# Performance work log

Hardware: AMD Instinct MI355X
Metric: run time of the kernel (lower is better)

Reference implementation:

```python
import jax, jax.numpy as jnp
import numpy as np

N_QUBITS = 12
N_LAYERS = 3
FEAT_DIM = 64
BATCH = 8192
PI = float(np.pi)


def setup_inputs() -> dict:
    key = jax.random.key(0)
    k1, k2, k3 = jax.random.split(key, 3)
    x = jax.random.normal(k1, (BATCH, FEAT_DIM), dtype=jnp.float32)
    # nn.Linear(feature_dim, num_qubits, bias=False) weight: [num_qubits, feature_dim]
    W = jax.random.normal(k2, (N_QUBITS, FEAT_DIM), dtype=jnp.float32) * (1.0 / np.sqrt(FEAT_DIM))
    # quantum params ~ Uniform(-pi, pi), shape [num_layers, num_qubits, 2] (RY, RZ angles)
    quantum_params = jax.random.uniform(k3, (N_LAYERS, N_QUBITS, 2), minval=-PI, maxval=PI, dtype=jnp.float32)
    return {"x": x, "W": W, "quantum_params": quantum_params}


def _halves(st, ax):
    a0 = jax.lax.index_in_dim(st, 0, ax, keepdims=True)
    a1 = jax.lax.index_in_dim(st, 1, ax, keepdims=True)
    return a0, a1


def _ry(st, theta, q, n):
    # RY(t) = [[cos t/2, -sin t/2], [sin t/2, cos t/2]] on qubit q (wire 0 = most significant)
    ax = q + 1
    c = jnp.cos(theta * 0.5)
    s = jnp.sin(theta * 0.5)
    if jnp.ndim(c) > 0:  # per-batch angles -> broadcast [B,1,...,1]
        c = c.reshape(c.shape + (1,) * n)
        s = s.reshape(s.shape + (1,) * n)
    a0, a1 = _halves(st, ax)
    return jnp.concatenate([c * a0 - s * a1, s * a0 + c * a1], axis=ax)


def _rz(st, theta, q, n):
    # RZ(t) = diag(e^{-i t/2}, e^{i t/2}) on qubit q
    ax = q + 1
    ph = jnp.exp(-0.5j * theta)
    a0, a1 = _halves(st, ax)
    return jnp.concatenate([ph * a0, jnp.conj(ph) * a1], axis=ax)


def _cnot(st, ctrl, tgt):
    # flip target amplitudes on the control=1 subspace
    ax_c, ax_t = ctrl + 1, tgt + 1
    s0, s1 = _halves(st, ax_c)
    return jnp.concatenate([s0, jnp.flip(s1, axis=ax_t)], axis=ax_c)


def reference(x, W, quantum_params):
    n = N_QUBITS
    # feature projection + tanh squashing to [-pi, pi]
    angles = jnp.tanh(x @ W.T) * PI  # [B, n]
    B = x.shape[0]
    # batched state vector |0...0>, shape [B] + [2]*n (wire 0 most significant, PennyLane convention)
    st = jnp.zeros((B,) + (2,) * n, dtype=jnp.complex64)
    st = st.at[(slice(None),) + (0,) * n].set(1.0)
    for layer in range(N_LAYERS):
        # data (re)uploading: RY(features[i]) each layer since data_reuploading=True
        for q in range(n):
            st = _ry(st, angles[:, q], q, n)
        # variational rotations
        for q in range(n):
            st = _ry(st, quantum_params[layer, q, 0], q, n)
            st = _rz(st, quantum_params[layer, q, 1], q, n)
        # ring entanglement
        for q in range(n):
            st = _cnot(st, q, (q + 1) % n)
    probs = jnp.real(st * jnp.conj(st))  # [B] + [2]*n
    outs = []
    for q in range(n):  # <PauliZ_q> = p(bit_q=0) - p(bit_q=1)
        axes = tuple(a for a in range(1, n + 1) if a != q + 1)
        p = probs.sum(axis=axes)  # [B, 2]
        outs.append(p[:, 0] - p[:, 1])
    return jnp.stack(outs, axis=1).astype(x.dtype)  # [B, n]
```

## Files before the change

kernel.cpp:

```cpp
#include <hip/hip_runtime.h>

namespace {

constexpr int NQ = 12;
constexpr int NL = 3;
constexpr int FEAT = 64;
constexpr float PI_F = 3.14159265358979323846f;

typedef float f2 __attribute__((ext_vector_type(2)));

struct Maps {
  unsigned m[NL][NQ];
  unsigned rv[NL][NQ];
  unsigned rf[NQ];
  bool ok;
};

constexpr Maps compute_raw() {
  Maps mp{};
  unsigned col[NQ] = {}, row[NQ] = {};
  for (int b = 0; b < NQ; ++b) { col[b] = 1u << b; row[b] = 1u << b; }
  mp.ok = true;
  for (int L = 0; L < NL; ++L) {
    for (int q = 0; q < NQ; ++q) {
      mp.m[L][q]  = col[NQ - 1 - q];
      mp.rv[L][q] = row[NQ - 1 - q];
      unsigned x = mp.m[L][q] & mp.rv[L][q];
      int pc = 0;
      for (int i = 0; i < NQ; ++i) pc ^= (int)((x >> i) & 1u);
      if (pc != 1) mp.ok = false;
    }
    for (int q = 0; q < NQ; ++q) {
      int bc = NQ - 1 - q;
      int bt = NQ - 1 - ((q + 1) % NQ);
      col[bc] ^= col[bt];
      row[bt] ^= row[bc];
    }
  }
  for (int q = 0; q < NQ; ++q) mp.rf[q] = row[NQ - 1 - q];
  return mp;
}

constexpr int pc12(unsigned x) { int c = 0; for (int i = 0; i < 12; ++i) c += (int)((x >> i) & 1u); return c; }

constexpr unsigned pmask(unsigned m, const int* pos) {
  unsigned r = 0;
  for (int b = 0; b < 12; ++b) if ((m >> b) & 1u) r |= 1u << pos[b];
  return r;
}

constexpr Maps compute_maps() {
  Maps raw = compute_raw();
  unsigned bestS = 0xFC0u; int best = -1;
  for (unsigned S = 0; S < 4096; ++S) {
    if (pc12(S) != 6) continue;
    int cnt = 0;
    for (int L = 0; L < NL; ++L)
      for (int q = 0; q < NQ; ++q)
        if ((raw.m[L][q] & ~S) == 0u) ++cnt;
    if (cnt > best) { best = cnt; bestS = S; }
  }
  int pos[12] = {};
  int lo = 0, hi = 6;
  for (int b = 0; b < 12; ++b) {
    if ((bestS >> b) & 1u) pos[b] = hi++; else pos[b] = lo++;
  }
  Maps mp{};
  mp.ok = raw.ok;
  for (int L = 0; L < NL; ++L)
    for (int q = 0; q < NQ; ++q) {
      mp.m[L][q]  = pmask(raw.m[L][q], pos);
      mp.rv[L][q] = pmask(raw.rv[L][q], pos);
    }
  for (int q = 0; q < NQ; ++q) mp.rf[q] = pmask(raw.rf[q], pos);
  return mp;
}

constexpr Maps MP = compute_maps();
static_assert(MP.ok, "pairing invariant violated");

__device__ __forceinline__ f2 pk_mul_bl(f2 a, f2 u) {
  f2 d;
  asm("v_pk_mul_f32 %0, %1, %2 op_sel:[0,0] op_sel_hi:[1,0]" : "=v"(d) : "v"(a), "v"(u));
  return d;
}
__device__ __forceinline__ f2 pk_fma_rot_p(f2 a, f2 u, f2 c) {
  f2 d;
  asm("v_pk_fma_f32 %0, %1, %2, %3 op_sel:[1,1,0] op_sel_hi:[0,1,1] neg_lo:[1,0,0]"
      : "=v"(d) : "v"(a), "v"(u), "v"(c));
  return d;
}
__device__ __forceinline__ f2 pk_fma_rot_m(f2 a, f2 u, f2 c) {
  f2 d;
  asm("v_pk_fma_f32 %0, %1, %2, %3 op_sel:[1,1,0] op_sel_hi:[0,1,1] neg_hi:[1,0,0]"
      : "=v"(d) : "v"(a), "v"(u), "v"(c));
  return d;
}
__device__ __forceinline__ f2 pk_fma_bl_p(f2 p, f2 v, f2 c) {
  f2 d;
  asm("v_pk_fma_f32 %0, %1, %2, %3 op_sel:[0,0,0] op_sel_hi:[1,0,1]"
      : "=v"(d) : "v"(p), "v"(v), "v"(c));
  return d;
}
__device__ __forceinline__ f2 pk_fma_bl_m(f2 p, f2 v, f2 c) {
  f2 d;
  asm("v_pk_fma_f32 %0, %1, %2, %3 op_sel:[0,0,0] op_sel_hi:[1,0,1] neg_lo:[0,1,0] neg_hi:[0,1,0]"
      : "=v"(d) : "v"(p), "v"(v), "v"(c));
  return d;
}
__device__ __forceinline__ f2 pk_mul_d(f2 a, f2 b) {
  f2 d;
  asm("v_pk_mul_f32 %0, %1, %2" : "=v"(d) : "v"(a), "v"(b));
  return d;
}
__device__ __forceinline__ f2 pk_fma_d(f2 a, f2 b, f2 c) {
  f2 d;
  asm("v_pk_fma_f32 %0, %1, %2, %3" : "=v"(d) : "v"(a), "v"(b), "v"(c));
  return d;
}

template<bool REAL>
__device__ __forceinline__ f2 updp(f2 a, f2 p, f2 u, f2 v) {
  if constexpr (REAL) return pk_fma_bl_p(p, v, pk_mul_bl(a, u));
  else return pk_fma_rot_p(p, v, pk_fma_bl_p(p, v, pk_fma_rot_p(a, u, pk_mul_bl(a, u))));
}
template<bool REAL>
__device__ __forceinline__ f2 updm(f2 a, f2 p, f2 u, f2 v) {
  if constexpr (REAL) return pk_fma_bl_m(p, v, pk_mul_bl(a, u));
  else return pk_fma_rot_p(p, v, pk_fma_bl_m(p, v, pk_fma_rot_m(a, u, pk_mul_bl(a, u))));
}

template<unsigned MLO>
__device__ __forceinline__ float shx(float v, int lane4) {
  if constexpr (MLO == 0u) {
    return v;
  } else if constexpr (MLO < 32u) {
    constexpr int off = (int)((MLO << 10) | 0x1fu);
    return __int_as_float(__builtin_amdgcn_ds_swizzle(__float_as_int(v), off));
  } else {
    int addr = lane4 ^ (int)(MLO << 2);
    return __int_as_float(__builtin_amdgcn_ds_bpermute(addr, __float_as_int(v)));
  }
}

template<unsigned M, unsigned R, int NREG, bool REAL>
__device__ __forceinline__ void gate(f2* st, float ghalf, float phihalf, int lane, int lane4) {
  float s, c;
  __sincosf(ghalf, &s, &c);
  constexpr unsigned MHI = (M >> 6) & 63u;
  constexpr unsigned MLO = M & 63u;
  constexpr unsigned RHI = (R >> 6) & 63u;
  constexpr unsigned RLO = R & 63u;
  float sL = (__popc((int)(RLO & (unsigned)lane)) & 1) ? -1.f : 1.f;
  f2 u, v;
  if constexpr (REAL) {
    u.x = c;       u.y = 0.f;
    v.x = -s * sL; v.y = 0.f;
  } else {
    float sf, cf;
    __sincosf(phihalf, &sf, &cf);
    u.x = c * cf;         u.y = (-c * sf) * sL;
    v.x = (-s * cf) * sL; v.y = s * sf;
  }
  if constexpr (MLO == 0u) {
    constexpr unsigned TB = MHI & (~MHI + 1u);
    #pragma unroll
    for (int r = 0; r < NREG; ++r) {
      if ((r & (int)TB) == 0) {
        int r2 = r ^ (int)MHI;
        const bool rp = ((__builtin_popcount((unsigned)r & RHI)) & 1) != 0;
        f2 a = st[r], b = st[r2];
        st[r]  = rp ? updm<REAL>(a, b, u, v) : updp<REAL>(a, b, u, v);
        st[r2] = rp ? updp<REAL>(b, a, u, v) : updm<REAL>(b, a, u, v);
      }
    }
  } else if constexpr (MHI == 0u) {
    #pragma unroll
    for (int r = 0; r < NREG; ++r) {
      f2 p;
      p.x = shx<MLO>(st[r].x, lane4);
      p.y = shx<MLO>(st[r].y, lane4);
      const bool rp = ((__builtin_popcount((unsigned)r & RHI)) & 1) != 0;
      st[r] = rp ? updm<REAL>(st[r], p, u, v) : updp<REAL>(st[r], p, u, v);
    }
  } else {
    constexpr unsigned TB = MHI & (~MHI + 1u);
    #pragma unroll
    for (int r = 0; r < NREG; ++r) {
      if ((r & (int)TB) == 0) {
        int r2 = r ^ (int)MHI;
        f2 pa, pb;
        pa.x = shx<MLO>(st[r2].x, lane4);
        pa.y = shx<MLO>(st[r2].y, lane4);
        pb.x = shx<MLO>(st[r].x, lane4);
        pb.y = shx<MLO>(st[r].y, lane4);
        const bool rp  = ((__builtin_popcount((unsigned)r  & RHI)) & 1) != 0;
        const bool rp2 = ((__builtin_popcount((unsigned)r2 & RHI)) & 1) != 0;
        f2 a = st[r], b = st[r2];
        st[r]  = rp  ? updm<REAL>(a, pa, u, v) : updp<REAL>(a, pa, u, v);
        st[r2] = rp2 ? updm<REAL>(b, pb, u, v) : updp<REAL>(b, pb, u, v);
      }
    }
  }
}

template<int Q>
__device__ __forceinline__ void l0_lane(f2* st, const float* ang, const float* __restrict__ qp, int lane, int lane4) {
  if constexpr (Q < NQ) {
    constexpr unsigned M = MP.m[0][Q];
    if constexpr (M < 64u) {
      gate<M, MP.rv[0][Q], 1, false>(st, 0.5f * (ang[Q] + qp[Q * 2 + 0]), 0.5f * qp[Q * 2 + 1], lane, lane4);
    }
    l0_lane<Q + 1>(st, ang, qp, lane, lane4);
  }
}

template<int Q, unsigned DONE>
__device__ __forceinline__ void l0_reg(f2* st, const float* ang, const float* __restrict__ qp) {
  if constexpr (Q < NQ) {
    constexpr unsigned M = MP.m[0][Q];
    if constexpr (M >= 64u) {
      constexpr unsigned TB = (M >> 6) & 63u;
      float sh = 0.5f * (ang[Q] + qp[Q * 2 + 0]);
      float ph = 0.5f * qp[Q * 2 + 1];
      float s, c, sf, cf;
      __sincosf(sh, &s, &c);
      __sincosf(ph, &sf, &cf);
      f2 u0; u0.x = c * cf; u0.y = -c * sf;
      f2 u1; u1.x = s * cf; u1.y = s * sf;
      #pragma unroll
      for (int r = 0; r < 64; ++r) {
        if ((r & ~(int)DONE & 63) == 0) {
          f2 a = st[r];
          int r2 = r | (int)TB;
          st[r]  = pk_fma_rot_p(a, u0, pk_mul_bl(a, u0));
          st[r2] = pk_fma_rot_p(a, u1, pk_mul_bl(a, u1));
        }
      }
      l0_reg<Q + 1, DONE | TB>(st, ang, qp);
    } else {
      l0_reg<Q + 1, DONE>(st, ang, qp);
    }
  }
}

template<int L, int Q>
__device__ __forceinline__ void do_gates(f2* st, const float* ang, const float* __restrict__ qp, int lane, int lane4) {
  if constexpr (Q == NQ) {
    if constexpr (L + 1 < NL) do_gates<L + 1, 0>(st, ang, qp, lane, lane4);
  } else {
    constexpr bool REAL = (L == NL - 1);
    float th0 = qp[(L * NQ + Q) * 2 + 0];
    float ph = REAL ? 0.f : 0.5f * qp[(L * NQ + Q) * 2 + 1];
    gate<MP.m[L][Q], MP.rv[L][Q], 64, REAL>(st, 0.5f * (ang[Q] + th0), ph, lane, lane4);
    do_gates<L, Q + 1>(st, ang, qp, lane, lane4);
  }
}

__device__ __forceinline__ float redsum(float v, int lane4) {
  v += shx<1>(v, lane4);
  v += shx<2>(v, lane4);
  v += shx<4>(v, lane4);
  v += shx<8>(v, lane4);
  v += shx<16>(v, lane4);
  v += shx<32>(v, lane4);
  return v;
}

__device__ __forceinline__ float fast_tanh(float x) {
  float e = __expf(2.f * x);
  float r = __builtin_amdgcn_rcpf(e + 1.f);
  return 1.f - 2.f * r;
}

template<int Q>
__device__ __forceinline__ void finish(const f2* acc6, float& outv, int lane, int lane4) {
  if constexpr (Q < NQ) {
    constexpr unsigned RLO = MP.rf[Q] & 63u;
    float a = (Q & 1) ? acc6[Q / 2].y : acc6[Q / 2].x;
    float sLn = (__popc((int)(RLO & (unsigned)lane)) & 1) ? -a : a;
    float t = redsum(sLn, lane4);
    if (lane == Q) outv = t;
    finish<Q + 1>(acc6, outv, lane, lane4);
  }
}

__global__ __launch_bounds__(64, 2) void qtr_kernel(const float* __restrict__ x,
                                                    const float* __restrict__ W,
                                                    const float* __restrict__ qp,
                                                    float* __restrict__ out) {
  int b = blockIdx.x;
  int lane = threadIdx.x;
  int lane4 = lane << 2;

  float xv = x[b * FEAT + lane];
  float ang[NQ];
  #pragma unroll
  for (int q = 0; q < NQ; ++q) {
    float prod = redsum(xv * W[q * FEAT + lane], lane4);
    ang[q] = PI_F * fast_tanh(prod);
  }

  f2 st[64];
  st[0].x = (lane == 0) ? 1.f : 0.f;
  st[0].y = 0.f;

  l0_lane<0>(st, ang, qp, lane, lane4);
  l0_reg<0, 0u>(st, ang, qp);
  do_gates<1, 0>(st, ang, qp, lane, lane4);

  f2 acc6[6];
  #pragma unroll
  for (int j = 0; j < 6; ++j) { acc6[j].x = 0.f; acc6[j].y = 0.f; }
  #pragma unroll
  for (int r = 0; r < 64; ++r) {
    f2 q2 = pk_mul_d(st[r], st[r]);
    float p = q2.x + q2.y;
    f2 pp; pp.x = p; pp.y = p;
    #pragma unroll
    for (int j = 0; j < 6; ++j) {
      const bool n0 = ((__builtin_popcount(((MP.rf[2 * j]     >> 6) & 63u) & (unsigned)r)) & 1) != 0;
      const bool n1 = ((__builtin_popcount(((MP.rf[2 * j + 1] >> 6) & 63u) & (unsigned)r)) & 1) != 0;
      f2 sg; sg.x = n0 ? -1.f : 1.f; sg.y = n1 ? -1.f : 1.f;
      acc6[j] = pk_fma_d(pp, sg, acc6[j]);
    }
  }

  float outv = 0.f;
  finish<0>(acc6, outv, lane, lane4);

  if (lane < NQ) out[b * NQ + lane] = outv;
}

}

extern "C" void kernel_launch(void* const* d_in, const int* in_sizes, int n_in,
                              void* d_out, int out_size, void* d_ws, size_t ws_size,
                              hipStream_t stream) {
  const float* x  = (const float*)d_in[0];
  const float* W  = (const float*)d_in[1];
  const float* qp = (const float*)d_in[2];
  float* out = (float*)d_out;
  qtr_kernel<<<8192, 64, 0, stream>>>(x, W, qp, out);
}
```

Measured before the change: 161.3 us.

## Remap state layout via LDS per six-gate phase so gates act on register bits

```diff
diff --git a/kernel.cpp b/kernel.cpp
--- a/kernel.cpp
+++ b/kernel.cpp
@@ -9,15 +9,56 @@
 
 typedef float f2 __attribute__((ext_vector_type(2)));
 
-struct Maps {
-  unsigned m[NL][NQ];
-  unsigned rv[NL][NQ];
-  unsigned rf[NQ];
+constexpr int par12(unsigned x) { int p = 0; for (int i = 0; i < 12; ++i) p ^= (int)((x >> i) & 1u); return p; }
+constexpr int lead12(unsigned x) { for (int k = 11; k >= 0; --k) if ((x >> k) & 1u) return k; return -1; }
+
+struct Ech { unsigned v[16]; int n; };
+constexpr unsigned ech_reduce(const Ech& E, unsigned x) {
+  for (int i = 0; i < E.n; ++i) {
+    int lb = lead12(E.v[i]);
+    if (lb >= 0 && ((x >> lb) & 1u)) x ^= E.v[i];
+  }
+  return x;
+}
+constexpr bool ech_add(Ech& E, unsigned x) {
+  unsigned r = ech_reduce(E, x);
+  if (!r) return false;
+  int lb = lead12(r);
+  int pos = E.n;
+  for (int i = 0; i < E.n; ++i) { if (lead12(E.v[i]) < lb) { pos = i; break; } }
+  for (int i = E.n; i > pos; --i) E.v[i] = E.v[i - 1];
+  E.v[pos] = r;
+  E.n++;
+  return true;
+}
+
+constexpr unsigned apmat(const unsigned* rows, unsigned v) {
+  unsigned o = 0; for (int k = 0; k < 12; ++k) if (par12(rows[k] & v)) o |= 1u << k; return o;
+}
+constexpr bool inv12(const unsigned* in, unsigned* out) {
+  unsigned a[12] = {}, b[12] = {};
+  for (int k = 0; k < 12; ++k) { a[k] = in[k]; b[k] = 1u << k; }
+  for (int c = 0; c < 12; ++c) {
+    int p = -1;
+    for (int r = c; r < 12; ++r) if ((a[r] >> c) & 1u) { p = r; break; }
+    if (p < 0) return false;
+    unsigned t = a[c]; a[c] = a[p]; a[p] = t; t = b[c]; b[c] = b[p]; b[p] = t;
+    for (int r = 0; r < 12; ++r) if (r != c && ((a[r] >> c) & 1u)) { a[r] ^= a[c]; b[r] ^= b[c]; }
+  }
+  for (int k = 0; k < 12; ++k) out[k] = b[k];
+  return true;
+}
+constexpr unsigned dropb(unsigned x, int t) {
+  unsigned lm = (1u << t) - 1u;
+  return (x & lm) | ((x >> 1) & (0x7FFu & ~lm));
+}
+
+struct Logical {
+  unsigned m[NL][NQ], rv[NL][NQ], rf[NQ];
   bool ok;
 };
-
-constexpr Maps compute_raw() {
-  Maps mp{};
+constexpr Logical compute_raw() {
+  Logical mp{};
   unsigned col[NQ] = {}, row[NQ] = {};
   for (int b = 0; b < NQ; ++b) { col[b] = 1u << b; row[b] = 1u << b; }
   mp.ok = true;
@@ -25,10 +66,7 @@
     for (int q = 0; q < NQ; ++q) {
       mp.m[L][q]  = col[NQ - 1 - q];
       mp.rv[L][q] = row[NQ - 1 - q];
-      unsigned x = mp.m[L][q] & mp.rv[L][q];
-      int pc = 0;
-      for (int i = 0; i < NQ; ++i) pc ^= (int)((x >> i) & 1u);
-      if (pc != 1) mp.ok = false;
+      if (par12(mp.m[L][q] & mp.rv[L][q]) != 1) mp.ok = false;
     }
     for (int q = 0; q < NQ; ++q) {
       int bc = NQ - 1 - q;
@@ -41,43 +79,147 @@
   return mp;
 }
 
-constexpr int pc12(unsigned x) { int c = 0; for (int i = 0; i < 12; ++i) c += (int)((x >> i) & 1u); return c; }
-
-constexpr unsigned pmask(unsigned m, const int* pos) {
-  unsigned r = 0;
-  for (int b = 0; b < 12; ++b) if ((m >> b) & 1u) r |= 1u << pos[b];
-  return r;
-}
-
-constexpr Maps compute_maps() {
-  Maps raw = compute_raw();
-  unsigned bestS = 0xFC0u; int best = -1;
-  for (unsigned S = 0; S < 4096; ++S) {
-    if (pc12(S) != 6) continue;
-    int cnt = 0;
-    for (int L = 0; L < NL; ++L)
-      for (int q = 0; q < NQ; ++q)
-        if ((raw.m[L][q] & ~S) == 0u) ++cnt;
-    if (cnt > best) { best = cnt; bestS = S; }
-  }
-  int pos[12] = {};
-  int lo = 0, hi = 6;
-  for (int b = 0; b < 12; ++b) {
-    if ((bestS >> b) & 1u) pos[b] = hi++; else pos[b] = lo++;
-  }
-  Maps mp{};
-  mp.ok = raw.ok;
-  for (int L = 0; L < NL; ++L)
-    for (int q = 0; q < NQ; ++q) {
-      mp.m[L][q]  = pmask(raw.m[L][q], pos);
-      mp.rv[L][q] = pmask(raw.rv[L][q], pos);
-    }
-  for (int q = 0; q < NQ; ++q) mp.rf[q] = pmask(raw.rf[q], pos);
-  return mp;
-}
-
-constexpr Maps MP = compute_maps();
-static_assert(MP.ok, "pairing invariant violated");
+struct Plan {
+  unsigned l0m[NQ], l0r[NQ];
+  unsigned gm[4][6];
+  unsigned gr[4][6];
+  unsigned rf[NQ];
+  unsigned phi[4][6];
+  unsigned coffE[4][64];
+  int cb[4];
+  bool ok;
+};
+
+constexpr bool findH(const Ech& G, unsigned rho, unsigned& out) {
+  for (unsigned t = 0; t < 12; ++t) {
+    unsigned v = 1u << t;
+    if (par12(v & rho) == 0 && ech_reduce(G, v)) { out = v; return true; }
+  }
+  for (unsigned v = 1; v < 4096u; ++v) {
+    if (par12(v & rho) == 0 && ech_reduce(G, v)) { out = v; return true; }
+  }
+  return false;
+}
+
+constexpr Plan build_plan() {
+  Logical raw = compute_raw();
+  Plan P{};
+  P.ok = raw.ok;
+  for (int q = 0; q < NQ; ++q) { P.l0m[q] = raw.m[0][q]; P.l0r[q] = raw.rv[0][q]; }
+  unsigned fwd[12] = {}, invc[12] = {};
+  for (int k = 0; k < 12; ++k) { fwd[k] = 1u << k; invc[k] = 1u << k; }
+  for (int ph = 0; ph < 4; ++ph) {
+    const int L = 1 + ph / 2, q0 = (ph % 2) * 6;
+    unsigned ml[6] = {};
+    for (int i = 0; i < 6; ++i) ml[i] = raw.m[L][q0 + i];
+    bool done = false;
+    for (int cbi = 5; cbi >= 0 && !done; --cbi) {
+      unsigned rho = fwd[6 + cbi];
+      bool bad = false;
+      int idx = -1;
+      for (int i = 0; i < 6; ++i) if (par12(ml[i] & rho)) { idx = i; break; }
+      unsigned uc = 0;
+      Ech W{};
+      if (idx >= 0) {
+        uc = ml[idx];
+        for (int i = 0; i < 6; ++i) {
+          if (i == idx) continue;
+          unsigned w = par12(ml[i] & rho) ? (ml[i] ^ uc) : ml[i];
+          ech_add(W, w);
+        }
+        if (W.n > 5) bad = true;
+      } else {
+        for (int i = 0; i < 6; ++i) ech_add(W, ml[i]);
+        if (W.n > 5) bad = true;
+        if (!bad) {
+          bool got = false;
+          for (unsigned t = 0; t < 12 && !got; ++t) {
+            unsigned v = 1u << t;
+            if (par12(v & rho)) { uc = v; got = true; }
+          }
+          if (!got) bad = true;
+        }
+      }
+      if (bad) continue;
+      Ech G{};
+      for (int i = 0; i < W.n && !bad; ++i) if (!ech_add(G, W.v[i])) bad = true;
+      if (!bad && !ech_add(G, uc)) bad = true;
+      if (bad) continue;
+      unsigned regH[5] = {};
+      int nH = W.n;
+      for (int i = 0; i < nH; ++i) regH[i] = W.v[i];
+      for (int slot = nH; slot < 5 && !bad; ++slot) {
+        unsigned v = 0;
+        if (!findH(G, rho, v)) { bad = true; break; }
+        regH[slot] = v; ech_add(G, v);
+      }
+      if (bad) continue;
+      unsigned lam[6] = {};
+      for (int j = 0; j < 6 && !bad; ++j) {
+        unsigned cand = invc[j];
+        if (par12(cand & rho) != 0 || !ech_reduce(G, cand)) {
+          if (!findH(G, rho, cand)) { bad = true; break; }
+        }
+        lam[j] = cand; ech_add(G, cand);
+      }
+      if (bad) continue;
+      unsigned ncols[12] = {};
+      for (int j = 0; j < 6; ++j) ncols[j] = lam[j];
+      {
+        int w = 0;
+        for (int k = 0; k < 6; ++k) ncols[6 + k] = (k == cbi) ? uc : regH[w++];
+      }
+      unsigned Mrows[12] = {};
+      for (int k = 0; k < 12; ++k) {
+        unsigned r = 0;
+        for (int j = 0; j < 12; ++j) r |= ((ncols[j] >> k) & 1u) << j;
+        Mrows[k] = r;
+      }
+      unsigned fnew[12] = {};
+      if (!inv12(Mrows, fnew)) continue;
+      bool okp = true;
+      unsigned gmv[6] = {}, grv[6] = {};
+      for (int i = 0; i < 6 && okp; ++i) {
+        unsigned SM = apmat(fnew, ml[i]);
+        if (SM & 63u) okp = false;
+        unsigned sg = 0;
+        for (int k = 0; k < 12; ++k) if (par12(raw.rv[L][q0 + i] & ncols[k])) sg |= 1u << k;
+        if (par12(SM & sg) != 1) okp = false;
+        gmv[i] = SM; grv[i] = sg;
+      }
+      unsigned phj[6] = {}, Ust[6] = {};
+      for (int j = 0; j < 6 && okp; ++j) {
+        phj[j] = apmat(fwd, lam[j]);
+        if ((phj[j] >> (6 + cbi)) & 1u) okp = false;
+      }
+      for (int k = 0; k < 6 && okp; ++k) {
+        Ust[k] = apmat(fwd, ncols[6 + k]);
+        if (((Ust[k] >> (6 + cbi)) & 1u) != (unsigned)(k == cbi ? 1 : 0)) okp = false;
+      }
+      if (!okp) continue;
+      P.cb[ph] = cbi;
+      for (int j = 0; j < 6; ++j) P.phi[ph][j] = phj[j];
+      for (int rp = 0; rp < 64; ++rp) {
+        unsigned psi = 0;
+        for (int k = 0; k < 6; ++k) if ((rp >> k) & 1) psi ^= Ust[k];
+        P.coffE[ph][rp] = dropb(psi, 6 + cbi);
+      }
+      for (int i = 0; i < 6; ++i) { P.gm[ph][i] = gmv[i]; P.gr[ph][i] = grv[i]; }
+      for (int k = 0; k < 12; ++k) { fwd[k] = fnew[k]; invc[k] = ncols[k]; }
+      done = true;
+    }
+    if (!done) { P.ok = false; return P; }
+  }
+  for (int q = 0; q < NQ; ++q) {
+    unsigned sg = 0;
+    for (int k = 0; k < 12; ++k) if (par12(raw.rf[q] & invc[k])) sg |= 1u << k;
+    P.rf[q] = sg;
+  }
+  return P;
+}
+
+constexpr Plan PLAN = build_plan();
+static_assert(PLAN.ok, "plan construction failed");
 
 __device__ __forceinline__ f2 pk_mul_bl(f2 a, f2 u) {
   f2 d;
@@ -174,7 +316,7 @@
         st[r2] = rp ? updp<REAL>(b, a, u, v) : updm<REAL>(b, a, u, v);
       }
     }
-  } else if constexpr (MHI == 0u) {
+  } else {
     #pragma unroll
     for (int r = 0; r < NREG; ++r) {
       f2 p;
@@ -183,42 +325,23 @@
       const bool rp = ((__builtin_popcount((unsigned)r & RHI)) & 1) != 0;
       st[r] = rp ? updm<REAL>(st[r], p, u, v) : updp<REAL>(st[r], p, u, v);
     }
-  } else {
-    constexpr unsigned TB = MHI & (~MHI + 1u);
-    #pragma unroll
-    for (int r = 0; r < NREG; ++r) {
-      if ((r & (int)TB) == 0) {
-        int r2 = r ^ (int)MHI;
-        f2 pa, pb;
-        pa.x = shx<MLO>(st[r2].x, lane4);
-        pa.y = shx<MLO>(st[r2].y, lane4);
-        pb.x = shx<MLO>(st[r].x, lane4);
-        pb.y = shx<MLO>(st[r].y, lane4);
-        const bool rp  = ((__builtin_popcount((unsigned)r  & RHI)) & 1) != 0;
-        const bool rp2 = ((__builtin_popcount((unsigned)r2 & RHI)) & 1) != 0;
-        f2 a = st[r], b = st[r2];
-        st[r]  = rp  ? updm<REAL>(a, pa, u, v) : updp<REAL>(a, pa, u, v);
-        st[r2] = rp2 ? updm<REAL>(b, pb, u, v) : updp<REAL>(b, pb, u, v);
-      }
-    }
   }
 }
 
 template<int Q>
 __device__ __forceinline__ void l0_lane(f2* st, const float* ang, const float* __restrict__ qp, int lane, int lane4) {
   if constexpr (Q < NQ) {
-    constexpr unsigned M = MP.m[0][Q];
+    constexpr unsigned M = PLAN.l0m[Q];
     if constexpr (M < 64u) {
-      gate<M, MP.rv[0][Q], 1, false>(st, 0.5f * (ang[Q] + qp[Q * 2 + 0]), 0.5f * qp[Q * 2 + 1], lane, lane4);
+      gate<M, PLAN.l0r[Q], 1, false>(st, 0.5f * (ang[Q] + qp[Q * 2 + 0]), 0.5f * qp[Q * 2 + 1], lane, lane4);
     }
     l0_lane<Q + 1>(st, ang, qp, lane, lane4);
   }
 }
-
 template<int Q, unsigned DONE>
 __device__ __forceinline__ void l0_reg(f2* st, const float* ang, const float* __restrict__ qp) {
   if constexpr (Q < NQ) {
-    constexpr unsigned M = MP.m[0][Q];
+    constexpr unsigned M = PLAN.l0m[Q];
     if constexpr (M >= 64u) {
       constexpr unsigned TB = (M >> 6) & 63u;
       float sh = 0.5f * (ang[Q] + qp[Q * 2 + 0]);
@@ -244,16 +367,47 @@
   }
 }
 
-template<int L, int Q>
-__device__ __forceinline__ void do_gates(f2* st, const float* ang, const float* __restrict__ qp, int lane, int lane4) {
-  if constexpr (Q == NQ) {
-    if constexpr (L + 1 < NL) do_gates<L + 1, 0>(st, ang, qp, lane, lane4);
-  } else {
+template<int PH>
+__device__ __forceinline__ void remap(f2* st, f2* lds, int lane) {
+  constexpr int b = PLAN.cb[PH];
+  constexpr unsigned LM6 = (1u << b) - 1u;
+  constexpr unsigned LM = (1u << (6 + b)) - 1u;
+  unsigned B = 0;
+  #pragma unroll
+  for (int j = 0; j < 6; ++j) B ^= (unsigned)(-(int)((lane >> j) & 1)) & PLAN.phi[PH][j];
+  unsigned rBe = (B & LM) | ((B >> 1) & (0x7FFu & ~LM));
+  #pragma unroll
+  for (int s = 0; s < 2; ++s) {
+    #pragma unroll
+    for (int r = 0; r < 64; ++r) {
+      if (((r >> b) & 1) == s) {
+        const int cr = (r & (int)LM6) | ((r >> 1) & (31 & ~(int)LM6));
+        lds[(cr << 6) | lane] = st[r];
+      }
+    }
+    asm volatile("s_waitcnt lgkmcnt(0)" ::: "memory");
+    #pragma unroll
+    for (int rp = 0; rp < 64; ++rp) {
+      if (((rp >> b) & 1) == s) {
+        st[rp] = lds[rBe ^ PLAN.coffE[PH][rp]];
+      }
+    }
+    asm volatile("s_waitcnt lgkmcnt(0)" ::: "memory");
+  }
+}
+
+template<int PH, int I>
+__device__ __forceinline__ void do_phase(f2* st, const float* ang, const float* __restrict__ qp, int lane, int lane4) {
+  if constexpr (I < 6) {
+    constexpr int L = 1 + PH / 2;
     constexpr bool REAL = (L == NL - 1);
-    float th0 = qp[(L * NQ + Q) * 2 + 0];
-    float ph = REAL ? 0.f : 0.5f * qp[(L * NQ + Q) * 2 + 1];
-    gate<MP.m[L][Q], MP.rv[L][Q], 64, REAL>(st, 0.5f * (ang[Q] + th0), ph, lane, lane4);
-    do_gates<L, Q + 1>(st, ang, qp, lane, lane4);
+    constexpr int q = (PH % 2) * 6 + I;
+    constexpr unsigned M = PLAN.gm[PH][I];
+    constexpr unsigned R = PLAN.gr[PH][I];
+    float th0 = qp[(L * NQ + q) * 2 + 0];
+    float ph1 = REAL ? 0.f : 0.5f * qp[(L * NQ + q) * 2 + 1];
+    gate<M, R, 64, REAL>(st, 0.5f * (ang[q] + th0), ph1, lane, lane4);
+    do_phase<PH, I + 1>(st, ang, qp, lane, lane4);
   }
 }
 
@@ -266,7 +420,6 @@
   v += shx<32>(v, lane4);
   return v;
 }
-
 __device__ __forceinline__ float fast_tanh(float x) {
   float e = __expf(2.f * x);
   float r = __builtin_amdgcn_rcpf(e + 1.f);
@@ -276,7 +429,7 @@
 template<int Q>
 __device__ __forceinline__ void finish(const f2* acc6, float& outv, int lane, int lane4) {
   if constexpr (Q < NQ) {
-    constexpr unsigned RLO = MP.rf[Q] & 63u;
+    constexpr unsigned RLO = PLAN.rf[Q] & 63u;
     float a = (Q & 1) ? acc6[Q / 2].y : acc6[Q / 2].x;
     float sLn = (__popc((int)(RLO & (unsigned)lane)) & 1) ? -a : a;
     float t = redsum(sLn, lane4);
@@ -289,6 +442,7 @@
                                                     const float* __restrict__ W,
                                                     const float* __restrict__ qp,
                                                     float* __restrict__ out) {
+  __shared__ f2 ldsb[2048];
   int b = blockIdx.x;
   int lane = threadIdx.x;
   int lane4 = lane << 2;
@@ -307,7 +461,15 @@
 
   l0_lane<0>(st, ang, qp, lane, lane4);
   l0_reg<0, 0u>(st, ang, qp);
-  do_gates<1, 0>(st, ang, qp, lane, lane4);
+
+  remap<0>(st, ldsb, lane);
+  do_phase<0, 0>(st, ang, qp, lane, lane4);
+  remap<1>(st, ldsb, lane);
+  do_phase<1, 0>(st, ang, qp, lane, lane4);
+  remap<2>(st, ldsb, lane);
+  do_phase<2, 0>(st, ang, qp, lane, lane4);
+  remap<3>(st, ldsb, lane);
+  do_phase<3, 0>(st, ang, qp, lane, lane4);
 
   f2 acc6[6];
   #pragma unroll
@@ -319,8 +481,8 @@
     f2 pp; pp.x = p; pp.y = p;
     #pragma unroll
     for (int j = 0; j < 6; ++j) {
-      const bool n0 = ((__builtin_popcount(((MP.rf[2 * j]     >> 6) & 63u) & (unsigned)r)) & 1) != 0;
-      const bool n1 = ((__builtin_popcount(((MP.rf[2 * j + 1] >> 6) & 63u) & (unsigned)r)) & 1) != 0;
+      const bool n0 = ((__builtin_popcount(((PLAN.rf[2 * j]     >> 6) & 63u) & (unsigned)r)) & 1) != 0;
+      const bool n1 = ((__builtin_popcount(((PLAN.rf[2 * j + 1] >> 6) & 63u) & (unsigned)r)) & 1) != 0;
       f2 sg; sg.x = n0 ? -1.f : 1.f; sg.y = n1 ? -1.f : 1.f;
       acc6[j] = pk_fma_d(pp, sg, acc6[j]);
     }
```

New measurement: 135.5 us. 16.0% less time.
